# Performance work log

Hardware: AMD Instinct MI355X
Metric: run time of the kernel (lower is better)

## Reference

```python
import jax, jax.numpy as jnp
import numpy as np

# LIF constants from __init__ defaults and forward body
TAU = 20.0        # membrane time constant
TH = 1.0          # base threshold
TAU_ADAPT = 100.0 # adaptation time constant
BETA_ADAPT = 1.5  # adaptation strength
V_RESET = -0.5    # reset potential
K = 10.0          # surrogate sigmoid slope


def setup_inputs() -> dict:
    key = jax.random.key(0)
    I = jax.random.normal(key, (16384, 2048), dtype=jnp.float32)
    return {"I": I}


def reference(I):
    # I: (B, L). Sequential LIF recurrence over L via lax.scan.
    B, L = I.shape
    dtype = I.dtype

    def step(carry, I_t):
        v, a, s_num = carry  # each (B,)
        th_eff = TH + BETA_ADAPT * a
        v = v - v / TAU + I_t  # v += dv
        s_soft = jax.nn.sigmoid(K * (v - th_eff))
        s_hard = (v >= th_eff).astype(dtype)
        # straight-through: forward value = s_hard, grad flows via s_soft
        s = jax.lax.stop_gradient(s_hard - s_soft) + s_soft
        s_num = s_num + s
        s_det = jax.lax.stop_gradient(s)  # reset is non-differentiable (detached)
        v = v * (1.0 - s_det) + V_RESET * s_det
        a = a - a / TAU_ADAPT + s
        return (v, a, s_num), (s, s_num)

    zeros = jnp.zeros((B,), dtype)
    _, (spikes_t, series_t) = jax.lax.scan(step, (zeros, zeros, zeros), I.T)
    # scan outputs are (L, B); transpose back to (B, L)
    return spikes_t.T, series_t.T
```

## Files before the change

kernel.cpp:

```cpp
#include <hip/hip_runtime.h>


#define LIF_L  2048
#define TILE   64
#define NTILES (LIF_L / TILE)

typedef float f32x2 __attribute__((ext_vector_type(2)));

constexpr float kR20 = -0.5f / 20.0f;
constexpr float kC0  = -0.5f - kR20;

__device__ __forceinline__ void barrier_lds_only() {
    asm volatile("s_waitcnt lgkmcnt(0)\n\ts_barrier" ::: "memory");
}

__device__ __forceinline__ float lif_step(float Inext, f32x2& x, float& th,
                                          float& carry) {
    const f32x2 C1 = {0.05f, 0.01f};
    const f32x2 C2 = {-20.0f, -100.0f};
    const f32x2 M1 = {-1.0f, -1.0f};
    bool fire = (x.x >= th);
    float s = fire ? 1.0f : 0.0f;
    f32x2 q   = x * C1;
    f32x2 r   = __builtin_elementwise_fma(C2, q, x);
    f32x2 d   = __builtin_elementwise_fma(r, C1, q);
    f32x2 dec = __builtin_elementwise_fma(d, M1, x);
    dec.x = fire ? kC0 : dec.x;
    f32x2 t = {Inext, s};
    x = dec + t;
    carry = __fadd_rn(carry, s);
    th = __fadd_rn(1.0f, __fmul_rn(1.5f, x.y));
    return s;
}

__device__ __forceinline__ int sw_idx(int row, int g) {
    return row * 64 + (((g) ^ (row & 15)) << 2);
}

__global__ __launch_bounds__(192, 1) void lif_fwd(const float* __restrict__ I,
                                                  float* __restrict__ spikes,
                                                  float* __restrict__ series) {
    __shared__ float sp_tile[4][64 * 64];
    __shared__ float se_tile[4][64 * 64];

    const int tid  = threadIdx.x;
    const int wave = tid >> 6;
    const int lane = tid & 63;
    const int row0 = blockIdx.x * 64;

    const float4* __restrict__ I4 =
        reinterpret_cast<const float4*>(I + (size_t)(row0 + lane) * LIF_L);

    f32x2 x = {0.0f, 0.0f};
    float th = 1.0f, carry = 0.0f;
    float4 bufA[16], bufB[16];

    if (wave == 0) {
        #pragma unroll
        for (int i = 0; i < 16; ++i) bufA[i] = I4[i];
        #pragma unroll
        for (int i = 0; i < 16; ++i) bufB[i] = I4[16 + i];
    }

    auto compute_tile = [&](const float4* buf, float nx0, float* sp, float* se) {
        #pragma unroll
        for (int c = 0; c < 16; ++c) {
            float4 in = buf[c];
            float nxt = (c < 15) ? buf[c + 1].x : nx0;
            float4 os, oc;
            os.x = lif_step(in.y, x, th, carry); oc.x = carry;
            os.y = lif_step(in.z, x, th, carry); oc.y = carry;
            os.z = lif_step(in.w, x, th, carry); oc.z = carry;
            os.w = lif_step(nxt,  x, th, carry); oc.w = carry;
            *reinterpret_cast<float4*>(&sp[sw_idx(lane, c)]) = os;
            *reinterpret_cast<float4*>(&se[sw_idx(lane, c)]) = oc;
        }
    };

    auto flush_tile = [&](int tkt, const float* sp, const float* se) {
        const size_t colbase = (size_t)tkt * TILE;
        #pragma unroll
        for (int i = 0; i < 16; ++i) {
            int row = i * 4 + (lane >> 4);
            int g   = lane & 15;
            int ix  = sw_idx(row, g);
            float4 vs = *reinterpret_cast<const float4*>(&sp[ix]);
            float4 ve = *reinterpret_cast<const float4*>(&se[ix]);
            size_t gaddr = (size_t)(row0 + row) * LIF_L + colbase + (size_t)g * 4;
            *reinterpret_cast<float4*>(spikes + gaddr) = vs;
            *reinterpret_cast<float4*>(series + gaddr) = ve;
        }
    };

    if (wave == 0) x.x = bufA[0].x;

    for (int p = 0; p < NTILES / 2; ++p) {
        const int kt = 2 * p;
        if (wave == 0) {
            compute_tile(bufA, bufB[0].x, sp_tile[kt & 3], se_tile[kt & 3]);
            if (kt + 2 < NTILES) {
                #pragma unroll
                for (int i = 0; i < 16; ++i) bufA[i] = I4[(kt + 2) * 16 + i];
            }
            float nx0 = (kt + 2 < NTILES) ? bufA[0].x : 0.0f;
            compute_tile(bufB, nx0, sp_tile[(kt + 1) & 3], se_tile[(kt + 1) & 3]);
            if (kt + 3 < NTILES) {
                #pragma unroll
                for (int i = 0; i < 16; ++i) bufB[i] = I4[(kt + 3) * 16 + i];
            }
        } else if (p > 0) {
            if (wave == 1) {
                flush_tile(kt - 2, sp_tile[(kt - 2) & 3], se_tile[(kt - 2) & 3]);
            } else {
                flush_tile(kt - 1, sp_tile[(kt - 1) & 3], se_tile[(kt - 1) & 3]);
            }
        }
        barrier_lds_only();
    }
    if (wave == 1) {
        flush_tile(NTILES - 2, sp_tile[(NTILES - 2) & 3], se_tile[(NTILES - 2) & 3]);
    } else if (wave == 2) {
        flush_tile(NTILES - 1, sp_tile[(NTILES - 1) & 3], se_tile[(NTILES - 1) & 3]);
    }
}

extern "C" void kernel_launch(void* const* d_in, const int* in_sizes, int n_in,
                              void* d_out, int out_size, void* d_ws, size_t ws_size,
                              hipStream_t stream) {
    const float* I = (const float*)d_in[0];
    const int B = in_sizes[0] / LIF_L;
    float* spikes = (float*)d_out;
    float* series = (float*)d_out + (size_t)B * LIF_L;

    const int threads = 192;
    const int blocks = B / 64;
    lif_fwd<<<blocks, threads, 0, stream>>>(I, spikes, series);
}
```

Measured before the change: 375.4 us.

## Drop LDS transpose staging and write outputs directly from compute wave

Removes the shared-memory tiles, the two flush waves and the per-tile barriers, so the single compute wave stores its spike and cumulative-count float4 values straight to global memory row by row. This cuts LDS traffic, barrier stalls and the extra waves per block. In exchange, each lane writes a different row, so global stores are strided by the row length rather than coalesced across lanes, and the stores now sit on the serial compute wave's critical path instead of being overlapped by helper waves.

```diff
diff --git a/kernel.cpp b/kernel.cpp
--- a/kernel.cpp
+++ b/kernel.cpp
@@ -9,10 +9,6 @@
 
 constexpr float kR20 = -0.5f / 20.0f;
 constexpr float kC0  = -0.5f - kR20;
-
-__device__ __forceinline__ void barrier_lds_only() {
-    asm volatile("s_waitcnt lgkmcnt(0)\n\ts_barrier" ::: "memory");
-}
 
 __device__ __forceinline__ float lif_step(float Inext, f32x2& x, float& th,
                                           float& carry) {
@@ -33,36 +29,29 @@
     return s;
 }
 
-__device__ __forceinline__ int sw_idx(int row, int g) {
-    return row * 64 + (((g) ^ (row & 15)) << 2);
-}
-
-__global__ __launch_bounds__(192, 1) void lif_fwd(const float* __restrict__ I,
-                                                  float* __restrict__ spikes,
-                                                  float* __restrict__ series) {
-    __shared__ float sp_tile[4][64 * 64];
-    __shared__ float se_tile[4][64 * 64];
-
-    const int tid  = threadIdx.x;
-    const int wave = tid >> 6;
-    const int lane = tid & 63;
-    const int row0 = blockIdx.x * 64;
+__global__ __launch_bounds__(64, 1) void lif_fwd(const float* __restrict__ I,
+                                                 float* __restrict__ spikes,
+                                                 float* __restrict__ series) {
+    const int lane = threadIdx.x;
+    const int row  = blockIdx.x * 64 + lane;
 
     const float4* __restrict__ I4 =
-        reinterpret_cast<const float4*>(I + (size_t)(row0 + lane) * LIF_L);
+        reinterpret_cast<const float4*>(I + (size_t)row * LIF_L);
+    float4* __restrict__ sp4 =
+        reinterpret_cast<float4*>(spikes + (size_t)row * LIF_L);
+    float4* __restrict__ se4 =
+        reinterpret_cast<float4*>(series + (size_t)row * LIF_L);
 
     f32x2 x = {0.0f, 0.0f};
     float th = 1.0f, carry = 0.0f;
     float4 bufA[16], bufB[16];
 
-    if (wave == 0) {
-        #pragma unroll
-        for (int i = 0; i < 16; ++i) bufA[i] = I4[i];
-        #pragma unroll
-        for (int i = 0; i < 16; ++i) bufB[i] = I4[16 + i];
-    }
+    #pragma unroll
+    for (int i = 0; i < 16; ++i) bufA[i] = I4[i];
+    #pragma unroll
+    for (int i = 0; i < 16; ++i) bufB[i] = I4[16 + i];
 
-    auto compute_tile = [&](const float4* buf, float nx0, float* sp, float* se) {
+    auto compute_tile = [&](const float4* buf, float nx0, int kt) {
         #pragma unroll
         for (int c = 0; c < 16; ++c) {
             float4 in = buf[c];
@@ -72,55 +61,26 @@
             os.y = lif_step(in.z, x, th, carry); oc.y = carry;
             os.z = lif_step(in.w, x, th, carry); oc.z = carry;
             os.w = lif_step(nxt,  x, th, carry); oc.w = carry;
-            *reinterpret_cast<float4*>(&sp[sw_idx(lane, c)]) = os;
-            *reinterpret_cast<float4*>(&se[sw_idx(lane, c)]) = oc;
+            sp4[kt * 16 + c] = os;
+            se4[kt * 16 + c] = oc;
         }
     };
 
-    auto flush_tile = [&](int tkt, const float* sp, const float* se) {
-        const size_t colbase = (size_t)tkt * TILE;
-        #pragma unroll
-        for (int i = 0; i < 16; ++i) {
-            int row = i * 4 + (lane >> 4);
-            int g   = lane & 15;
-            int ix  = sw_idx(row, g);
-            float4 vs = *reinterpret_cast<const float4*>(&sp[ix]);
-            float4 ve = *reinterpret_cast<const float4*>(&se[ix]);
-            size_t gaddr = (size_t)(row0 + row) * LIF_L + colbase + (size_t)g * 4;
-            *reinterpret_cast<float4*>(spikes + gaddr) = vs;
-            *reinterpret_cast<float4*>(series + gaddr) = ve;
-        }
-    };
-
-    if (wave == 0) x.x = bufA[0].x;
+    x.x = bufA[0].x;
 
     for (int p = 0; p < NTILES / 2; ++p) {
         const int kt = 2 * p;
-        if (wave == 0) {
-            compute_tile(bufA, bufB[0].x, sp_tile[kt & 3], se_tile[kt & 3]);
-            if (kt + 2 < NTILES) {
-                #pragma unroll
-                for (int i = 0; i < 16; ++i) bufA[i] = I4[(kt + 2) * 16 + i];
-            }
-            float nx0 = (kt + 2 < NTILES) ? bufA[0].x : 0.0f;
-            compute_tile(bufB, nx0, sp_tile[(kt + 1) & 3], se_tile[(kt + 1) & 3]);
-            if (kt + 3 < NTILES) {
-                #pragma unroll
-                for (int i = 0; i < 16; ++i) bufB[i] = I4[(kt + 3) * 16 + i];
-            }
-        } else if (p > 0) {
-            if (wave == 1) {
-                flush_tile(kt - 2, sp_tile[(kt - 2) & 3], se_tile[(kt - 2) & 3]);
-            } else {
-                flush_tile(kt - 1, sp_tile[(kt - 1) & 3], se_tile[(kt - 1) & 3]);
-            }
+        compute_tile(bufA, bufB[0].x, kt);
+        if (kt + 2 < NTILES) {
+            #pragma unroll
+            for (int i = 0; i < 16; ++i) bufA[i] = I4[(kt + 2) * 16 + i];
         }
-        barrier_lds_only();
-    }
-    if (wave == 1) {
-        flush_tile(NTILES - 2, sp_tile[(NTILES - 2) & 3], se_tile[(NTILES - 2) & 3]);
-    } else if (wave == 2) {
-        flush_tile(NTILES - 1, sp_tile[(NTILES - 1) & 3], se_tile[(NTILES - 1) & 3]);
+        float nx0 = (kt + 2 < NTILES) ? bufA[0].x : 0.0f;
+        compute_tile(bufB, nx0, kt + 1);
+        if (kt + 3 < NTILES) {
+            #pragma unroll
+            for (int i = 0; i < 16; ++i) bufB[i] = I4[(kt + 3) * 16 + i];
+        }
     }
 }
 
@@ -132,7 +92,7 @@
     float* spikes = (float*)d_out;
     float* series = (float*)d_out + (size_t)B * LIF_L;
 
-    const int threads = 192;
+    const int threads = 64;
     const int blocks = B / 64;
     lif_fwd<<<blocks, threads, 0, stream>>>(I, spikes, series);
 }
```

Measured after the change: 407.4 us. 1.09x slower.

## Move spike cumulative sum off the serial wave into a separate pipeline stage

Applied to the files above, without the earlier changes.

The running spike-count accumulation leaves the serial recurrence wave. Wave 0 now only computes spikes. Wave 1 reads the spike tiles from LDS, forms the prefix sum into the series tiles, and wave 2 streams both outputs to global memory with a one-stage lag for the series. This shortens the per-step dependency chain and cuts LDS stores on the critical wave. In exchange it adds a pipeline stage, more LDS traffic on the helper waves, and puts all global stores on a single wave.

```diff
diff --git a/kernel.cpp b/kernel.cpp
--- a/kernel.cpp
+++ b/kernel.cpp
@@ -14,8 +14,7 @@
     asm volatile("s_waitcnt lgkmcnt(0)\n\ts_barrier" ::: "memory");
 }
 
-__device__ __forceinline__ float lif_step(float Inext, f32x2& x, float& th,
-                                          float& carry) {
+__device__ __forceinline__ float lif_step(float Inext, f32x2& x, float& th) {
     const f32x2 C1 = {0.05f, 0.01f};
     const f32x2 C2 = {-20.0f, -100.0f};
     const f32x2 M1 = {-1.0f, -1.0f};
@@ -25,10 +24,9 @@
     f32x2 r   = __builtin_elementwise_fma(C2, q, x);
     f32x2 d   = __builtin_elementwise_fma(r, C1, q);
     f32x2 dec = __builtin_elementwise_fma(d, M1, x);
-    dec.x = fire ? kC0 : dec.x;
-    f32x2 t = {Inext, s};
-    x = dec + t;
-    carry = __fadd_rn(carry, s);
+    float sel = fire ? kC0 : dec.x;
+    x.x = __fadd_rn(sel, Inext);
+    x.y = __fadd_rn(dec.y, s);
     th = __fadd_rn(1.0f, __fmul_rn(1.5f, x.y));
     return s;
 }
@@ -52,8 +50,9 @@
         reinterpret_cast<const float4*>(I + (size_t)(row0 + lane) * LIF_L);
 
     f32x2 x = {0.0f, 0.0f};
-    float th = 1.0f, carry = 0.0f;
+    float th = 1.0f;
     float4 bufA[16], bufB[16];
+    float carry = 0.0f;
 
     if (wave == 0) {
         #pragma unroll
@@ -62,33 +61,44 @@
         for (int i = 0; i < 16; ++i) bufB[i] = I4[16 + i];
     }
 
-    auto compute_tile = [&](const float4* buf, float nx0, float* sp, float* se) {
+    auto compute_tile = [&](const float4* buf, float nx0, float* sp) {
         #pragma unroll
         for (int c = 0; c < 16; ++c) {
             float4 in = buf[c];
             float nxt = (c < 15) ? buf[c + 1].x : nx0;
-            float4 os, oc;
-            os.x = lif_step(in.y, x, th, carry); oc.x = carry;
-            os.y = lif_step(in.z, x, th, carry); oc.y = carry;
-            os.z = lif_step(in.w, x, th, carry); oc.z = carry;
-            os.w = lif_step(nxt,  x, th, carry); oc.w = carry;
+            float4 os;
+            os.x = lif_step(in.y, x, th);
+            os.y = lif_step(in.z, x, th);
+            os.z = lif_step(in.w, x, th);
+            os.w = lif_step(nxt,  x, th);
             *reinterpret_cast<float4*>(&sp[sw_idx(lane, c)]) = os;
-            *reinterpret_cast<float4*>(&se[sw_idx(lane, c)]) = oc;
         }
     };
 
-    auto flush_tile = [&](int tkt, const float* sp, const float* se) {
+    auto cumsum_tile = [&](const float* sp, float* se) {
+        #pragma unroll
+        for (int c = 0; c < 16; ++c) {
+            int ix = sw_idx(lane, c);
+            float4 sv = *reinterpret_cast<const float4*>(&sp[ix]);
+            float4 nv;
+            carry = __fadd_rn(carry, sv.x); nv.x = carry;
+            carry = __fadd_rn(carry, sv.y); nv.y = carry;
+            carry = __fadd_rn(carry, sv.z); nv.z = carry;
+            carry = __fadd_rn(carry, sv.w); nv.w = carry;
+            *reinterpret_cast<float4*>(&se[ix]) = nv;
+        }
+    };
+
+    auto flush_stream = [&](int tkt, const float* buf, float* gbase) {
         const size_t colbase = (size_t)tkt * TILE;
         #pragma unroll
         for (int i = 0; i < 16; ++i) {
             int row = i * 4 + (lane >> 4);
             int g   = lane & 15;
             int ix  = sw_idx(row, g);
-            float4 vs = *reinterpret_cast<const float4*>(&sp[ix]);
-            float4 ve = *reinterpret_cast<const float4*>(&se[ix]);
+            float4 v = *reinterpret_cast<const float4*>(&buf[ix]);
             size_t gaddr = (size_t)(row0 + row) * LIF_L + colbase + (size_t)g * 4;
-            *reinterpret_cast<float4*>(spikes + gaddr) = vs;
-            *reinterpret_cast<float4*>(series + gaddr) = ve;
+            *reinterpret_cast<float4*>(gbase + gaddr) = v;
         }
     };
 
@@ -97,30 +107,48 @@
     for (int p = 0; p < NTILES / 2; ++p) {
         const int kt = 2 * p;
         if (wave == 0) {
-            compute_tile(bufA, bufB[0].x, sp_tile[kt & 3], se_tile[kt & 3]);
+            compute_tile(bufA, bufB[0].x, sp_tile[kt & 3]);
             if (kt + 2 < NTILES) {
                 #pragma unroll
                 for (int i = 0; i < 16; ++i) bufA[i] = I4[(kt + 2) * 16 + i];
             }
             float nx0 = (kt + 2 < NTILES) ? bufA[0].x : 0.0f;
-            compute_tile(bufB, nx0, sp_tile[(kt + 1) & 3], se_tile[(kt + 1) & 3]);
+            compute_tile(bufB, nx0, sp_tile[(kt + 1) & 3]);
             if (kt + 3 < NTILES) {
                 #pragma unroll
                 for (int i = 0; i < 16; ++i) bufB[i] = I4[(kt + 3) * 16 + i];
             }
-        } else if (p > 0) {
-            if (wave == 1) {
-                flush_tile(kt - 2, sp_tile[(kt - 2) & 3], se_tile[(kt - 2) & 3]);
-            } else {
-                flush_tile(kt - 1, sp_tile[(kt - 1) & 3], se_tile[(kt - 1) & 3]);
+        } else if (wave == 1) {
+            if (p > 0) {
+                cumsum_tile(sp_tile[(kt - 2) & 3], se_tile[(kt - 2) & 3]);
+                cumsum_tile(sp_tile[(kt - 1) & 3], se_tile[(kt - 1) & 3]);
+            }
+        } else {
+            if (p > 0) {
+                flush_stream(kt - 2, sp_tile[(kt - 2) & 3], spikes);
+                flush_stream(kt - 1, sp_tile[(kt - 1) & 3], spikes);
+            }
+            if (p > 1) {
+                flush_stream(kt - 4, se_tile[(kt - 4) & 3], series);
+                flush_stream(kt - 3, se_tile[(kt - 3) & 3], series);
             }
         }
         barrier_lds_only();
     }
     if (wave == 1) {
-        flush_tile(NTILES - 2, sp_tile[(NTILES - 2) & 3], se_tile[(NTILES - 2) & 3]);
+        cumsum_tile(sp_tile[2], se_tile[2]);
+        cumsum_tile(sp_tile[3], se_tile[3]);
     } else if (wave == 2) {
-        flush_tile(NTILES - 1, sp_tile[(NTILES - 1) & 3], se_tile[(NTILES - 1) & 3]);
+        flush_stream(NTILES - 2, sp_tile[2], spikes);
+        flush_stream(NTILES - 1, sp_tile[3], spikes);
+        flush_stream(NTILES - 4, se_tile[0], series);
+        flush_stream(NTILES - 3, se_tile[1], series);
+    }
+    barrier_lds_only();
+    if (wave == 1) {
+        flush_stream(NTILES - 2, se_tile[2], series);
+    } else if (wave == 2) {
+        flush_stream(NTILES - 1, se_tile[3], series);
     }
 }
 
```

Measured after the change: 376.7 us. No clear change (+0.4%).
